# Kernel optimization log

Measured on AMD Instinct MI355X. Metric: run time of the kernel, lower is better.

Reference implementation:

```python
import jax, jax.numpy as jnp
import numpy as np

D_MODEL = 1024
NUM_HEADS = 16
D_FF = 2688
BATCH = 2
SEQ = 2048
EPS = 1e-5


def _trunc_normal(key, shape, std):
    # truncated normal on [-3, 3] then scaled by std (matches trunc_normal_(mean=0,std,a=-3,b=3) approximately)
    return std * jax.random.truncated_normal(key, -3.0 / std if std > 0 else -3.0, 3.0 / std if std > 0 else 3.0, shape, jnp.float32) * std / std if False else jax.random.truncated_normal(key, -3.0, 3.0, shape, jnp.float32) * std


def setup_inputs() -> dict:
    key = jax.random.key(0)
    ks = jax.random.split(key, 8)
    def lin(k, d_out, d_in):
        std = (2.0 / (d_in + d_out)) ** 0.5
        return _trunc_normal(k, (d_out, d_in), std)
    return {
        "x": jax.random.normal(ks[0], (BATCH, SEQ, D_MODEL), jnp.float32),
        "wqkv": lin(ks[1], 3 * D_MODEL, D_MODEL),
        "wo": lin(ks[2], D_MODEL, D_MODEL),
        "g1": jnp.ones((D_MODEL,), jnp.float32),
        "g2": jnp.ones((D_MODEL,), jnp.float32),
        "w1": lin(ks[3], D_FF, D_MODEL),
        "w2": lin(ks[4], D_MODEL, D_FF),
        "w3": lin(ks[5], D_FF, D_MODEL),
    }


def _rmsnorm(x, g):
    rms = jnp.sqrt(jnp.mean(x * x, axis=-1, keepdims=True) + EPS)
    return x * (g / rms)


def _mhsa(x, wqkv, wo):
    B, S, D = x.shape
    H, Dk = NUM_HEADS, D // NUM_HEADS
    qkv = jnp.einsum('bsd,ed->bse', x, wqkv)  # [B,S,3D]
    q, k, v = jnp.split(qkv, 3, axis=-1)
    def heads(t):
        return t.reshape(B, S, H, Dk).transpose(0, 2, 1, 3)  # [B,H,S,Dk]
    q, k, v = heads(q), heads(k), heads(v)
    scores = jnp.einsum('bhqd,bhkd->bhqk', q, k) / jnp.sqrt(jnp.asarray(Dk, x.dtype))
    causal = jnp.tril(jnp.ones((S, S), bool))
    scores = jnp.where(causal, scores, -jnp.inf)
    attn = jax.nn.softmax(scores, axis=-1)
    out = jnp.einsum('bhqk,bhkd->bhqd', attn, v)
    out = out.transpose(0, 2, 1, 3).reshape(B, S, D)
    return jnp.einsum('bsd,ed->bse', out, wo)


def _swiglu(x, w1, w2, w3):
    a = jnp.einsum('bsd,fd->bsf', x, w1)
    b = jnp.einsum('bsd,fd->bsf', x, w3)
    h = (a * jax.nn.sigmoid(a)) * b
    return jnp.einsum('bsf,df->bsd', h, w2)


def reference(x, wqkv, wo, g1, g2, w1, w2, w3):
    x = x + _mhsa(_rmsnorm(x, g1), wqkv, wo)
    x = x + _swiglu(_rmsnorm(x, g2), w1, w2, w3)
    return x
```

## Files before the change

### kernel.cpp

```cpp
#include <hip/hip_runtime.h>
#include <cstdint>
#include <cstddef>

typedef unsigned short u16;
typedef __attribute__((ext_vector_type(8))) short short8;
typedef __attribute__((ext_vector_type(4))) float float4v;

struct alignas(8) u16x4 { u16 x, y, z, w; };

__device__ __forceinline__ float bf2f(u16 u) {
  union { uint32_t i; float f; } x;
  x.i = ((uint32_t)u) << 16;
  return x.f;
}
__device__ __forceinline__ u16 f2bf(float f) {
  union { float f; uint32_t i; } x;
  x.f = f;
  uint32_t r = x.i + 0x7fffu + ((x.i >> 16) & 1u);
  return (u16)(r >> 16);
}
__device__ __forceinline__ int4 pack8(const float4& a, const float4& b) {
  int4 r;
  r.x = (uint32_t)f2bf(a.x) | ((uint32_t)f2bf(a.y) << 16);
  r.y = (uint32_t)f2bf(a.z) | ((uint32_t)f2bf(a.w) << 16);
  r.z = (uint32_t)f2bf(b.x) | ((uint32_t)f2bf(b.y) << 16);
  r.w = (uint32_t)f2bf(b.z) | ((uint32_t)f2bf(b.w) << 16);
  return r;
}

__device__ __forceinline__ void gload_lds16(const void* g, void* l) {
  __builtin_amdgcn_global_load_lds(
      (const __attribute__((address_space(1))) void*)g,
      (__attribute__((address_space(3))) void*)l, 16, 0, 0);
}

#define WAITV_BAR(N)                                              \
  do {                                                            \
    asm volatile("s_waitcnt vmcnt(%0)" ::"n"(N) : "memory");      \
    __builtin_amdgcn_s_barrier();                                 \
    __builtin_amdgcn_sched_barrier(0);                            \
  } while (0)

#define BAR_ONLY()                                                \
  do {                                                            \
    __builtin_amdgcn_sched_barrier(0);                            \
    __builtin_amdgcn_s_barrier();                                 \
    __builtin_amdgcn_sched_barrier(0);                            \
  } while (0)

#define LGKM0_FENCE()                                             \
  do {                                                            \
    asm volatile("s_waitcnt lgkmcnt(0)" ::: "memory");            \
    __builtin_amdgcn_sched_barrier(0);                            \
  } while (0)

__device__ __forceinline__ int2 xcd_swizzle_xmajor() {
  const int gx = gridDim.x, gy = gridDim.y;
  const int nwg = gx * gy;
  const int lin = blockIdx.x + blockIdx.y * gx;
  const int nl = (lin & 7) * (nwg >> 3) + (lin >> 3);
  const int bx = nl / gy;
  const int by = nl - bx * gy;
  return make_int2(bx, by);
}

struct PrepArgs {
  const float* src[5];
  u16* dst[5];
  int pre[6];
};

__global__ __launch_bounds__(256) void prep_kernel(PrepArgs a)
{
  const int g = blockIdx.x * 256 + threadIdx.x;
  if (g >= a.pre[5]) return;
  int t = 0;
#pragma unroll
  for (int i = 0; i < 5; i++) if (g >= a.pre[i + 1]) t = i + 1;
  const int idx = (g - a.pre[t]) * 8;
  const float* s = a.src[t] + idx;
  float4 v0 = *(const float4*)(s);
  float4 v1 = *(const float4*)(s + 4);
  *(int4*)(a.dst[t] + idx) = pack8(v0, v1);
}

template <int RMODE, bool OUTF32, int TN>
__global__ __launch_bounds__(256) void gemm_bt_kernel(
    const u16* __restrict__ A, const u16* __restrict__ B,
    void* __restrict__ Cv, const void* __restrict__ Rv,
    int M, int N, int K)
{
  constexpr int JN = TN / 32;
  constexpr int NLD = (TN == 128) ? 4 : 3;
  __shared__ u16 As[3][128 * 32];
  __shared__ u16 Bs[3][TN * 32];
  const int t = threadIdx.x;
  const int lane = t & 63;
  const int wave = t >> 6;
  const int l15 = lane & 15;
  const int quad = lane >> 4;
  const int wm = (wave >> 1) * 64;
  const int wn = (wave & 1) * (TN / 2);
  const int2 bb = xcd_swizzle_xmajor();
  const int m0 = bb.y * 128;
  const int n0 = bb.x * TN;
  const int sw = quad ^ ((l15 >> 1) & 3);

  float4v acc[4][JN] = {};

  const int r0 = t >> 2, q0s = (t & 3) ^ ((t >> 3) & 3);
  const int s1 = 256 + t;
  const int r1 = s1 >> 2, q1s = (s1 & 3) ^ ((s1 >> 3) & 3);

  auto stage = [&](int bi, int kk) {
    gload_lds16(A + (size_t)(m0 + r0) * K + kk + q0s * 8, &As[bi][(wave * 64) * 8]);
    gload_lds16(A + (size_t)(m0 + r1) * K + kk + q1s * 8, &As[bi][(256 + wave * 64) * 8]);
    gload_lds16(B + (size_t)(n0 + r0) * K + kk + q0s * 8, &Bs[bi][(wave * 64) * 8]);
    if (TN == 128)
      gload_lds16(B + (size_t)(n0 + r1) * K + kk + q1s * 8, &Bs[bi][(256 + wave * 64) * 8]);
  };
  auto compute = [&](int bi) {
    short8 af[4], bfr[JN];
#pragma unroll
    for (int i = 0; i < 4; i++)
      af[i] = *(const short8*)(&As[bi][((wm + i * 16 + l15) * 4 + sw) * 8]);
#pragma unroll
    for (int j = 0; j < JN; j++)
      bfr[j] = *(const short8*)(&Bs[bi][((wn + j * 16 + l15) * 4 + sw) * 8]);
#pragma unroll
    for (int i = 0; i < 4; i++)
#pragma unroll
      for (int j = 0; j < JN; j++)
        acc[i][j] = __builtin_amdgcn_mfma_f32_16x16x32_bf16(af[i], bfr[j], acc[i][j], 0, 0, 0);
  };

  const int nk = K >> 5;
  stage(0, 0);
  stage(1, 32);
  int bc = 0, bs = 2;
  for (int i = 0; i + 2 < nk; ++i) {
    stage(bs, (i + 2) << 5);
    WAITV_BAR(2 * NLD);
    compute(bc);
    BAR_ONLY();
    bc = (bc == 2) ? 0 : bc + 1;
    bs = (bs == 2) ? 0 : bs + 1;
  }
  WAITV_BAR(NLD);
  compute(bc);
  bc = (bc == 2) ? 0 : bc + 1;
  WAITV_BAR(0);
  compute(bc);

#pragma unroll
  for (int i = 0; i < 4; i++) {
#pragma unroll
    for (int r = 0; r < 4; r++) {
      const int row = m0 + wm + i * 16 + quad * 4 + r;
      const size_t base = (size_t)row * N;
#pragma unroll
      for (int j = 0; j < JN; j++) {
        const int col = n0 + wn + j * 16 + l15;
        float v = acc[i][j][r];
        if (RMODE == 1) v += ((const float*)Rv)[base + col];
        if (RMODE == 2) v += bf2f(((const u16*)Rv)[base + col]);
        if (OUTF32) ((float*)Cv)[base + col] = v;
        else        ((u16*)Cv)[base + col] = f2bf(v);
      }
    }
  }
}

__global__ __launch_bounds__(512) void gemm_w13_kernel(
    const u16* __restrict__ A, const u16* __restrict__ B1,
    const u16* __restrict__ B2, u16* __restrict__ C,
    int M, int N, int K)
{
  __shared__ u16 As[3][128 * 64];
  __shared__ u16 B1s[3][128 * 64];
  __shared__ u16 B2s[3][128 * 64];
  const int t = threadIdx.x;
  const int lane = t & 63;
  const int wave = t >> 6;
  const int l15 = lane & 15;
  const int quad = lane >> 4;
  const int wm = (wave >> 2) * 64;
  const int wn = (wave & 3) * 32;
  const int2 bb = xcd_swizzle_xmajor();
  const int m0 = bb.y * 128;
  const int n0 = bb.x * 128;

  float4v accA[4][2] = {};
  float4v accB[4][2] = {};

  const int sub = lane >> 3;
  const int slot = lane & 7;

  auto stageA = [&](int bi, int kt) {
#pragma unroll
    for (int j = 0; j < 2; j++) {
      const int r = j * 64 + wave * 8 + sub;
      gload_lds16(A + (size_t)(m0 + r) * K + kt + ((slot ^ (r & 7)) * 8),
                  &As[bi][j * 4096 + wave * 512]);
    }
  };
  auto stageB1 = [&](int bi, int kt) {
#pragma unroll
    for (int j = 0; j < 2; j++) {
      const int r = j * 64 + wave * 8 + sub;
      gload_lds16(B1 + (size_t)(n0 + r) * K + kt + ((slot ^ (r & 7)) * 8),
                  &B1s[bi][j * 4096 + wave * 512]);
    }
  };
  auto stageB2 = [&](int bi, int kt) {
#pragma unroll
    for (int j = 0; j < 2; j++) {
      const int r = j * 64 + wave * 8 + sub;
      gload_lds16(B2 + (size_t)(n0 + r) * K + kt + ((slot ^ (r & 7)) * 8),
                  &B2s[bi][j * 4096 + wave * 512]);
    }
  };

  const int nkt = K >> 6;
  stageA(0, 0);  stageB1(0, 0);  stageB2(0, 0);
  stageA(1, 64); stageB1(1, 64); stageB2(1, 64);
  WAITV_BAR(6);

  int cur = 0;
  for (int i = 0; i < nkt; ++i) {
    const int stg = (cur >= 1) ? cur - 1 : 2;
    const int kt2 = (i + 2) << 6;
    short8 af[4][2], b1f[2][2];
#pragma unroll
    for (int ii = 0; ii < 4; ii++) {
      const int R = wm + ii * 16 + l15;
#pragma unroll
      for (int ks = 0; ks < 2; ks++)
        af[ii][ks] = *(const short8*)(&As[cur][R * 64 + (((ks * 4 + quad) ^ (R & 7)) * 8)]);
    }
#pragma unroll
    for (int j = 0; j < 2; j++) {
      const int R = wn + j * 16 + l15;
#pragma unroll
      for (int ks = 0; ks < 2; ks++)
        b1f[j][ks] = *(const short8*)(&B1s[cur][R * 64 + (((ks * 4 + quad) ^ (R & 7)) * 8)]);
    }
    if (i + 2 < nkt) { stageA(stg, kt2); stageB1(stg, kt2); }
    __builtin_amdgcn_s_barrier();
    LGKM0_FENCE();
    __builtin_amdgcn_s_setprio(1);
#pragma unroll
    for (int ii = 0; ii < 4; ii++)
#pragma unroll
      for (int j = 0; j < 2; j++)
#pragma unroll
        for (int ks = 0; ks < 2; ks++)
          accA[ii][j] = __builtin_amdgcn_mfma_f32_16x16x32_bf16(af[ii][ks], b1f[j][ks], accA[ii][j], 0, 0, 0);
    __builtin_amdgcn_s_setprio(0);
    BAR_ONLY();
    short8 b2f[2][2];
#pragma unroll
    for (int j = 0; j < 2; j++) {
      const int R = wn + j * 16 + l15;
#pragma unroll
      for (int ks = 0; ks < 2; ks++)
        b2f[j][ks] = *(const short8*)(&B2s[cur][R * 64 + (((ks * 4 + quad) ^ (R & 7)) * 8)]);
    }
    if (i + 2 < nkt) stageB2(stg, kt2);
    __builtin_amdgcn_s_barrier();
    LGKM0_FENCE();
    __builtin_amdgcn_s_setprio(1);
#pragma unroll
    for (int ii = 0; ii < 4; ii++)
#pragma unroll
      for (int j = 0; j < 2; j++)
#pragma unroll
        for (int ks = 0; ks < 2; ks++)
          accB[ii][j] = __builtin_amdgcn_mfma_f32_16x16x32_bf16(af[ii][ks], b2f[j][ks], accB[ii][j], 0, 0, 0);
    __builtin_amdgcn_s_setprio(0);
    if (i + 2 < nkt)      WAITV_BAR(6);
    else if (i + 1 < nkt) WAITV_BAR(0);
    cur = (cur == 2) ? 0 : cur + 1;
  }

#pragma unroll
  for (int i = 0; i < 4; i++) {
#pragma unroll
    for (int r = 0; r < 4; r++) {
      const int row = m0 + wm + i * 16 + quad * 4 + r;
      const size_t base = (size_t)row * N;
#pragma unroll
      for (int j = 0; j < 2; j++) {
        const int col = n0 + wn + j * 16 + l15;
        float a = accA[i][j][r];
        float b = accB[i][j][r];
        float h = a / (1.f + __expf(-a)) * b;
        C[base + col] = f2bf(h);
      }
    }
  }
}

__global__ __launch_bounds__(256) void vtrans_kernel(
    const u16* __restrict__ qkv, u16* __restrict__ VtG)
{
  __shared__ u16 T[64 * 72];
  const int t = threadIdx.x;
  const int s0 = blockIdx.x * 64;
  const int bh = blockIdx.y, b = bh >> 4, h = bh & 15;
  {
    const int sl = t >> 2, dseg = (t & 3) * 16;
    const size_t src = ((size_t)b * 2048 + s0 + sl) * 3072 + 2048 + h * 64 + dseg;
    int4 v0 = *(const int4*)(qkv + src);
    int4 v1 = *(const int4*)(qkv + src + 8);
    *(int4*)(&T[sl * 72 + dseg]) = v0;
    *(int4*)(&T[sl * 72 + dseg + 8]) = v1;
  }
  __syncthreads();
  {
    const int d = t >> 2, sseg = (t & 3) * 16;
    alignas(16) u16 buf[16];
#pragma unroll
    for (int i = 0; i < 16; i++) buf[i] = T[(sseg + i) * 72 + d];
    u16* dst = VtG + ((size_t)bh * 64 + d) * 2048 + s0 + sseg;
    *(int4*)(dst) = *(const int4*)(&buf[0]);
    *(int4*)(dst + 8) = *(const int4*)(&buf[8]);
  }
}

__global__ __launch_bounds__(256) void attn_kernel(
    const u16* __restrict__ qkv, const u16* __restrict__ VtG,
    u16* __restrict__ outp)
{
  __shared__ u16 Ks[2][2][128 * 32];
  __shared__ u16 Vt[2][4][64 * 32];
  __shared__ u16 Pl[4][2048];
  const int t = threadIdx.x;
  const int lane = t & 63;
  const int wave = t >> 6;
  const int l15 = lane & 15;
  const int quad = lane >> 4;
  const int sw = quad ^ ((l15 >> 1) & 3);
  const int gx = gridDim.x;
  const int nwg = gx * gridDim.y;
  const int lin = blockIdx.x + blockIdx.y * gx;
  const int nl = (lin & 7) * (nwg >> 3) + (lin >> 3);
  const int bh = nl / gx;
  const int pair = nl - bh * gx;
  const int b = bh >> 4, h = bh & 15;
  const size_t srow = (size_t)b * 2048;
  const int rr = lane >> 2, qs = (lane & 3) ^ ((lane >> 3) & 3);
  u16* plw = Pl[wave];

  auto stageKV = [&](int bi, int ic) {
    const int c0 = ic * 128;
#pragma unroll
    for (int k = 0; k < 8; k++) {
      const int I = wave * 8 + k;
      if (I < 16) {
        const int half = I >> 3, rb = (I & 7) * 16, row = rb + rr;
        gload_lds16(qkv + (srow + c0 + row) * 3072 + 1024 + h * 64 + half * 32 + qs * 8,
                    &Ks[bi][half][rb * 32]);
      } else {
        const int g = (I - 16) >> 2, rb = ((I - 16) & 3) * 16, row = rb + rr;
        gload_lds16(VtG + ((size_t)bh * 64 + row) * 2048 + c0 + g * 32 + qs * 8,
                    &Vt[bi][g][rb * 32]);
      }
    }
  };

  for (int tsel = 0; tsel < 2; tsel++) {
    const int qt = tsel ? 31 - pair : pair;
    const int tq0 = qt * 64;
    const int q = tq0 + wave * 16 + l15;

    short8 qf[2];
    {
      const size_t qbase = (srow + q) * 3072 + h * 64;
#pragma unroll
      for (int dh = 0; dh < 2; dh++) {
        int4 raw = *(const int4*)(qkv + qbase + dh * 32 + quad * 8);
        const u16* rp = (const u16*)&raw;
        short8 f;
#pragma unroll
        for (int j = 0; j < 8; j++)
          ((u16*)&f)[j] = f2bf(bf2f(rp[j]) * 0.125f);
        qf[dh] = f;
      }
    }

    float m_i = -INFINITY, l_i = 0.f;
    float4v accO[4] = {};
    const int nc = (qt + 2) >> 1;

    stageKV(0, 0);
    for (int ic = 0; ic < nc; ic++) {
      const int cb = ic & 1;
      const int c0 = ic * 128;
      if (ic + 1 < nc) {
        stageKV(cb ^ 1, ic + 1);
        WAITV_BAR(8);
      } else {
        WAITV_BAR(0);
      }

      float4v accS[8];
#pragma unroll
      for (int ks = 0; ks < 8; ks++) {
        short8 kf0 = *(const short8*)(&Ks[cb][0][((ks * 16 + l15) * 4 + sw) * 8]);
        short8 kf1 = *(const short8*)(&Ks[cb][1][((ks * 16 + l15) * 4 + sw) * 8]);
        float4v z = {};
        z = __builtin_amdgcn_mfma_f32_16x16x32_bf16(kf0, qf[0], z, 0, 0, 0);
        accS[ks] = __builtin_amdgcn_mfma_f32_16x16x32_bf16(kf1, qf[1], z, 0, 0, 0);
      }

      if (ic == nc - 1) {
#pragma unroll
        for (int ks = 0; ks < 8; ks++)
#pragma unroll
          for (int r = 0; r < 4; r++)
            if (c0 + ks * 16 + quad * 4 + r > q) accS[ks][r] = -INFINITY;
      }

      float cmax = -INFINITY;
#pragma unroll
      for (int ks = 0; ks < 8; ks++)
#pragma unroll
        for (int r = 0; r < 4; r++) cmax = fmaxf(cmax, accS[ks][r]);
      cmax = fmaxf(cmax, __shfl_xor(cmax, 16));
      cmax = fmaxf(cmax, __shfl_xor(cmax, 32));
      const float mn = fmaxf(m_i, cmax);
      const float alpha = __expf(m_i - mn);

      float psum = 0.f;
#pragma unroll
      for (int ks = 0; ks < 8; ks++) {
        float p0 = __expf(accS[ks][0] - mn);
        float p1 = __expf(accS[ks][1] - mn);
        float p2 = __expf(accS[ks][2] - mn);
        float p3 = __expf(accS[ks][3] - mn);
        psum += (p0 + p1) + (p2 + p3);
        u16x4 pk;
        pk.x = f2bf(p0); pk.y = f2bf(p1); pk.z = f2bf(p2); pk.w = f2bf(p3);
        const int seg = ((ks & 1) * 2 + (quad >> 1)) ^ ((l15 >> 1) & 3);
        *(u16x4*)(&plw[(ks >> 1) * 512 + (l15 * 4 + seg) * 8 + (quad & 1) * 4]) = pk;
      }
      psum += __shfl_xor(psum, 16);
      psum += __shfl_xor(psum, 32);
      l_i = l_i * alpha + psum;
      m_i = mn;
#pragma unroll
      for (int ds = 0; ds < 4; ds++)
#pragma unroll
        for (int r = 0; r < 4; r++) accO[ds][r] *= alpha;

      __threadfence_block();

#pragma unroll
      for (int kh = 0; kh < 4; kh++) {
        short8 pf = *(const short8*)(&plw[kh * 512 + (l15 * 4 + sw) * 8]);
#pragma unroll
        for (int ds = 0; ds < 4; ds++) {
          short8 vf = *(const short8*)(&Vt[cb][kh][((ds * 16 + l15) * 4 + sw) * 8]);
          accO[ds] = __builtin_amdgcn_mfma_f32_16x16x32_bf16(vf, pf, accO[ds], 0, 0, 0);
        }
      }
      BAR_ONLY();
    }

    const float invl = 1.f / l_i;
    const size_t obase = (srow + q) * 1024 + h * 64;
#pragma unroll
    for (int ds = 0; ds < 4; ds++) {
      u16x4 pk;
      pk.x = f2bf(accO[ds][0] * invl);
      pk.y = f2bf(accO[ds][1] * invl);
      pk.z = f2bf(accO[ds][2] * invl);
      pk.w = f2bf(accO[ds][3] * invl);
      *(u16x4*)(outp + obase + ds * 16 + quad * 4) = pk;
    }
  }
}

template <bool XF32>
__global__ __launch_bounds__(256) void rmsnorm_kernel(
    const void* __restrict__ xv, const float* __restrict__ g, u16* __restrict__ o)
{
  const int row = blockIdx.x;
  const int t = threadIdx.x;
  float f0, f1, f2, f3;
  if (XF32) {
    float4 v = *(const float4*)((const float*)xv + (size_t)row * 1024 + t * 4);
    f0 = v.x; f1 = v.y; f2 = v.z; f3 = v.w;
  } else {
    int2 v = *(const int2*)((const u16*)xv + (size_t)row * 1024 + t * 4);
    const u16* p = (const u16*)&v;
    f0 = bf2f(p[0]); f1 = bf2f(p[1]); f2 = bf2f(p[2]); f3 = bf2f(p[3]);
  }
  float ss = f0 * f0 + f1 * f1 + f2 * f2 + f3 * f3;
#pragma unroll
  for (int off = 32; off > 0; off >>= 1) ss += __shfl_down(ss, off);
  __shared__ float red[4];
  if ((t & 63) == 0) red[t >> 6] = ss;
  __syncthreads();
  const float tot = red[0] + red[1] + red[2] + red[3];
  const float inv = rsqrtf(tot * (1.0f / 1024.0f) + 1e-5f);
  float4 gv = *(const float4*)(g + t * 4);
  u16x4 ov;
  ov.x = f2bf(f0 * gv.x * inv);
  ov.y = f2bf(f1 * gv.y * inv);
  ov.z = f2bf(f2 * gv.z * inv);
  ov.w = f2bf(f3 * gv.w * inv);
  *(u16x4*)(o + (size_t)row * 1024 + t * 4) = ov;
}

extern "C" void kernel_launch(void* const* d_in, const int* in_sizes, int n_in,
                              void* d_out, int out_size, void* d_ws, size_t ws_size,
                              hipStream_t stream)
{
  const float* x    = (const float*)d_in[0];
  const float* wqkv = (const float*)d_in[1];
  const float* wo   = (const float*)d_in[2];
  const float* g1   = (const float*)d_in[3];
  const float* g2   = (const float*)d_in[4];
  const float* w1   = (const float*)d_in[5];
  const float* w2   = (const float*)d_in[6];
  const float* w3   = (const float*)d_in[7];
  float* out = (float*)d_out;
  char* ws = (char*)d_ws;
  (void)in_sizes; (void)n_in; (void)out_size; (void)ws_size;

  size_t off = 0;
  auto alloc = [&](size_t bytes) { void* p = ws + off; off += (bytes + 255) & ~(size_t)255; return p; };
  u16* wqkvb = (u16*)alloc((size_t)3072 * 1024 * 2);
  u16* wob   = (u16*)alloc((size_t)1024 * 1024 * 2);
  u16* w1b   = (u16*)alloc((size_t)2688 * 1024 * 2);
  u16* w2b   = (u16*)alloc((size_t)2688 * 1024 * 2);
  u16* w3b   = (u16*)alloc((size_t)2688 * 1024 * 2);
  u16* S1    = (u16*)alloc((size_t)4096 * 1024 * 2);
  u16* S2    = (u16*)alloc((size_t)4096 * 3072 * 2);
  u16* S3    = (u16*)alloc((size_t)4096 * 1024 * 2);
  u16* VtG   = (u16*)alloc((size_t)32 * 64 * 2048 * 2);

  PrepArgs pa;
  const float* srcs[5] = {wqkv, wo, w1, w2, w3};
  u16* dsts[5] = {wqkvb, wob, w1b, w2b, w3b};
  const int nelem[5] = {3072 * 1024, 1024 * 1024, 2688 * 1024, 2688 * 1024, 2688 * 1024};
  int pre = 0;
  for (int i = 0; i < 5; i++) {
    pa.src[i] = srcs[i];
    pa.dst[i] = dsts[i];
    pa.pre[i] = pre;
    pre += nelem[i] / 8;
  }
  pa.pre[5] = pre;
  prep_kernel<<<(pre + 255) / 256, 256, 0, stream>>>(pa);

  rmsnorm_kernel<true><<<4096, 256, 0, stream>>>(x, g1, S1);
  gemm_bt_kernel<0, false, 128><<<dim3(24, 32), 256, 0, stream>>>(S1, wqkvb, S2,
                                                  nullptr, 4096, 3072, 1024);
  vtrans_kernel<<<dim3(32, 32), 256, 0, stream>>>(S2, VtG);
  attn_kernel<<<dim3(16, 32), 256, 0, stream>>>(S2, VtG, S1);
  gemm_bt_kernel<1, false, 64><<<dim3(16, 32), 256, 0, stream>>>(S1, wob, S3, x,
                                                  4096, 1024, 1024);
  rmsnorm_kernel<false><<<4096, 256, 0, stream>>>(S3, g2, S1);
  gemm_w13_kernel<<<dim3(21, 32), 512, 0, stream>>>(S1, w1b, w3b, S2,
                                                  4096, 2688, 1024);
  gemm_bt_kernel<2, true, 64><<<dim3(16, 32), 256, 0, stream>>>(S2, w2b, out, S3,
                                                  4096, 1024, 2688);
}
```

Baseline: 331.8 us.

## Rework generic GEMM into 512-thread 128x128x64 tiles with split-phase staging

Replaces the templated 256-thread GEMM (128xTN tiles, K-step 32) with a 512-thread 128x128 tile kernel using K-step 64, an XOR-swizzled LDS layout and a schedule that interleaves A and B staging between two MFMA half-steps, with s_setprio around the MFMA bursts. It is meant to cut barrier and wait overhead per K and improve overlap of global-to-LDS loads with compute, mirroring the w13 kernel design. The out-projection and down-projection GEMMs now launch half as many blocks (8x32 grid = 256 blocks), which may underfill the GPU's compute units, and LDS use per block rises substantially.

```diff
diff --git a/kernel.cpp b/kernel.cpp
--- a/kernel.cpp
+++ b/kernel.cpp
@@ -84,73 +84,103 @@
   *(int4*)(a.dst[t] + idx) = pack8(v0, v1);
 }
 
-template <int RMODE, bool OUTF32, int TN>
-__global__ __launch_bounds__(256) void gemm_bt_kernel(
+template <int RMODE, bool OUTF32>
+__global__ __launch_bounds__(512) void gemm_bt_kernel(
     const u16* __restrict__ A, const u16* __restrict__ B,
     void* __restrict__ Cv, const void* __restrict__ Rv,
     int M, int N, int K)
 {
-  constexpr int JN = TN / 32;
-  constexpr int NLD = (TN == 128) ? 4 : 3;
-  __shared__ u16 As[3][128 * 32];
-  __shared__ u16 Bs[3][TN * 32];
+  __shared__ u16 As[3][128 * 64];
+  __shared__ u16 Bs[3][128 * 64];
   const int t = threadIdx.x;
   const int lane = t & 63;
   const int wave = t >> 6;
   const int l15 = lane & 15;
   const int quad = lane >> 4;
-  const int wm = (wave >> 1) * 64;
-  const int wn = (wave & 1) * (TN / 2);
+  const int wm = (wave >> 2) * 64;
+  const int wn = (wave & 3) * 32;
   const int2 bb = xcd_swizzle_xmajor();
   const int m0 = bb.y * 128;
-  const int n0 = bb.x * TN;
-  const int sw = quad ^ ((l15 >> 1) & 3);
-
-  float4v acc[4][JN] = {};
-
-  const int r0 = t >> 2, q0s = (t & 3) ^ ((t >> 3) & 3);
-  const int s1 = 256 + t;
-  const int r1 = s1 >> 2, q1s = (s1 & 3) ^ ((s1 >> 3) & 3);
-
-  auto stage = [&](int bi, int kk) {
-    gload_lds16(A + (size_t)(m0 + r0) * K + kk + q0s * 8, &As[bi][(wave * 64) * 8]);
-    gload_lds16(A + (size_t)(m0 + r1) * K + kk + q1s * 8, &As[bi][(256 + wave * 64) * 8]);
-    gload_lds16(B + (size_t)(n0 + r0) * K + kk + q0s * 8, &Bs[bi][(wave * 64) * 8]);
-    if (TN == 128)
-      gload_lds16(B + (size_t)(n0 + r1) * K + kk + q1s * 8, &Bs[bi][(256 + wave * 64) * 8]);
+  const int n0 = bb.x * 128;
+
+  float4v acc[4][2] = {};
+
+  const int sub = lane >> 3;
+  const int slot = lane & 7;
+
+  auto stageA = [&](int bi, int kt) {
+#pragma unroll
+    for (int j = 0; j < 2; j++) {
+      const int r = j * 64 + wave * 8 + sub;
+      gload_lds16(A + (size_t)(m0 + r) * K + kt + ((slot ^ (r & 7)) * 8),
+                  &As[bi][j * 4096 + wave * 512]);
+    }
   };
-  auto compute = [&](int bi) {
-    short8 af[4], bfr[JN];
-#pragma unroll
-    for (int i = 0; i < 4; i++)
-      af[i] = *(const short8*)(&As[bi][((wm + i * 16 + l15) * 4 + sw) * 8]);
-#pragma unroll
-    for (int j = 0; j < JN; j++)
-      bfr[j] = *(const short8*)(&Bs[bi][((wn + j * 16 + l15) * 4 + sw) * 8]);
-#pragma unroll
-    for (int i = 0; i < 4; i++)
-#pragma unroll
-      for (int j = 0; j < JN; j++)
-        acc[i][j] = __builtin_amdgcn_mfma_f32_16x16x32_bf16(af[i], bfr[j], acc[i][j], 0, 0, 0);
+  auto stageB = [&](int bi, int kt) {
+#pragma unroll
+    for (int j = 0; j < 2; j++) {
+      const int r = j * 64 + wave * 8 + sub;
+      gload_lds16(B + (size_t)(n0 + r) * K + kt + ((slot ^ (r & 7)) * 8),
+                  &Bs[bi][j * 4096 + wave * 512]);
+    }
   };
 
-  const int nk = K >> 5;
-  stage(0, 0);
-  stage(1, 32);
-  int bc = 0, bs = 2;
-  for (int i = 0; i + 2 < nk; ++i) {
-    stage(bs, (i + 2) << 5);
-    WAITV_BAR(2 * NLD);
-    compute(bc);
+  const int nkt = K >> 6;
+  stageA(0, 0);  stageB(0, 0);
+  stageA(1, 64); stageB(1, 64);
+  WAITV_BAR(4);
+
+  int cur = 0;
+  for (int i = 0; i < nkt; ++i) {
+    const int stg = (cur >= 1) ? cur - 1 : 2;
+    const int kt2 = (i + 2) << 6;
+    short8 af0[4], bf0[2];
+#pragma unroll
+    for (int ii = 0; ii < 4; ii++) {
+      const int R = wm + ii * 16 + l15;
+      af0[ii] = *(const short8*)(&As[cur][R * 64 + ((quad ^ (R & 7)) * 8)]);
+    }
+#pragma unroll
+    for (int j = 0; j < 2; j++) {
+      const int R = wn + j * 16 + l15;
+      bf0[j] = *(const short8*)(&Bs[cur][R * 64 + ((quad ^ (R & 7)) * 8)]);
+    }
+    if (i + 2 < nkt) stageA(stg, kt2);
+    __builtin_amdgcn_s_barrier();
+    LGKM0_FENCE();
+    __builtin_amdgcn_s_setprio(1);
+#pragma unroll
+    for (int ii = 0; ii < 4; ii++)
+#pragma unroll
+      for (int j = 0; j < 2; j++)
+        acc[ii][j] = __builtin_amdgcn_mfma_f32_16x16x32_bf16(af0[ii], bf0[j], acc[ii][j], 0, 0, 0);
+    __builtin_amdgcn_s_setprio(0);
     BAR_ONLY();
-    bc = (bc == 2) ? 0 : bc + 1;
-    bs = (bs == 2) ? 0 : bs + 1;
-  }
-  WAITV_BAR(NLD);
-  compute(bc);
-  bc = (bc == 2) ? 0 : bc + 1;
-  WAITV_BAR(0);
-  compute(bc);
+    short8 af1[4], bf1[2];
+#pragma unroll
+    for (int ii = 0; ii < 4; ii++) {
+      const int R = wm + ii * 16 + l15;
+      af1[ii] = *(const short8*)(&As[cur][R * 64 + (((4 + quad) ^ (R & 7)) * 8)]);
+    }
+#pragma unroll
+    for (int j = 0; j < 2; j++) {
+      const int R = wn + j * 16 + l15;
+      bf1[j] = *(const short8*)(&Bs[cur][R * 64 + (((4 + quad) ^ (R & 7)) * 8)]);
+    }
+    if (i + 2 < nkt) stageB(stg, kt2);
+    __builtin_amdgcn_s_barrier();
+    LGKM0_FENCE();
+    __builtin_amdgcn_s_setprio(1);
+#pragma unroll
+    for (int ii = 0; ii < 4; ii++)
+#pragma unroll
+      for (int j = 0; j < 2; j++)
+        acc[ii][j] = __builtin_amdgcn_mfma_f32_16x16x32_bf16(af1[ii], bf1[j], acc[ii][j], 0, 0, 0);
+    __builtin_amdgcn_s_setprio(0);
+    if (i + 2 < nkt)      WAITV_BAR(4);
+    else if (i + 1 < nkt) WAITV_BAR(0);
+    cur = (cur == 2) ? 0 : cur + 1;
+  }
 
 #pragma unroll
   for (int i = 0; i < 4; i++) {
@@ -159,7 +189,7 @@
       const int row = m0 + wm + i * 16 + quad * 4 + r;
       const size_t base = (size_t)row * N;
 #pragma unroll
-      for (int j = 0; j < JN; j++) {
+      for (int j = 0; j < 2; j++) {
         const int col = n0 + wn + j * 16 + l15;
         float v = acc[i][j][r];
         if (RMODE == 1) v += ((const float*)Rv)[base + col];
@@ -557,15 +587,15 @@
   prep_kernel<<<(pre + 255) / 256, 256, 0, stream>>>(pa);
 
   rmsnorm_kernel<true><<<4096, 256, 0, stream>>>(x, g1, S1);
-  gemm_bt_kernel<0, false, 128><<<dim3(24, 32), 256, 0, stream>>>(S1, wqkvb, S2,
+  gemm_bt_kernel<0, false><<<dim3(24, 32), 512, 0, stream>>>(S1, wqkvb, S2,
                                                   nullptr, 4096, 3072, 1024);
   vtrans_kernel<<<dim3(32, 32), 256, 0, stream>>>(S2, VtG);
   attn_kernel<<<dim3(16, 32), 256, 0, stream>>>(S2, VtG, S1);
-  gemm_bt_kernel<1, false, 64><<<dim3(16, 32), 256, 0, stream>>>(S1, wob, S3, x,
+  gemm_bt_kernel<1, false><<<dim3(8, 32), 512, 0, stream>>>(S1, wob, S3, x,
                                                   4096, 1024, 1024);
   rmsnorm_kernel<false><<<4096, 256, 0, stream>>>(S3, g2, S1);
   gemm_w13_kernel<<<dim3(21, 32), 512, 0, stream>>>(S1, w1b, w3b, S2,
                                                   4096, 2688, 1024);
-  gemm_bt_kernel<2, true, 64><<<dim3(16, 32), 256, 0, stream>>>(S2, w2b, out, S3,
+  gemm_bt_kernel<2, true><<<dim3(8, 32), 512, 0, stream>>>(S2, w2b, out, S3,
                                                   4096, 1024, 2688);
 }
```

Result: no change. 335.2 us (+1.0%).
